# Kernel optimization log

Measured on AMD Instinct MI355X. Metric: run time of the kernel, lower is better.

Reference implementation:

```python
import jax, jax.numpy as jnp
import numpy as np

N_NODES = 100000
N_EDGES = 640000
HIDDEN = 128
OUT = 128


def _graph_conv(x, edge_index, W_rel, b_rel, W_root):
    # PyG GraphConv (aggr='add'):
    #   out[i] = x[i] @ W_root.T + (sum_{(j->i) in E} x[j]) @ W_rel.T + b_rel
    src, dst = edge_index[0], edge_index[1]
    agg = jax.ops.segment_sum(x[src], dst, num_segments=N_NODES)  # [N, d_in]
    return x @ W_root.T + agg @ W_rel.T + b_rel


def setup_inputs() -> dict:
    key = jax.random.key(0)
    ks = jax.random.split(key, 10)
    x = jax.random.normal(ks[0], (N_NODES, HIDDEN), dtype=jnp.float32)
    edge_index = jax.random.randint(ks[1], (2, N_EDGES), 0, N_NODES, dtype=jnp.int64)
    s = 1.0 / np.sqrt(HIDDEN)
    def w(k, o, i):
        return jax.random.normal(k, (o, i), dtype=jnp.float32) * s
    return {
        "x": x,
        "edge_index": edge_index,
        "W_rel0": w(ks[2], HIDDEN, HIDDEN), "b0": jnp.zeros((HIDDEN,), jnp.float32), "W_root0": w(ks[3], HIDDEN, HIDDEN),
        "W_rel1": w(ks[4], HIDDEN, HIDDEN), "b1": jnp.zeros((HIDDEN,), jnp.float32), "W_root1": w(ks[5], HIDDEN, HIDDEN),
        "W_rel2": w(ks[6], OUT, HIDDEN),    "b2": jnp.zeros((OUT,), jnp.float32),    "W_root2": w(ks[7], OUT, HIDDEN),
    }


def reference(x, edge_index, W_rel0, b0, W_root0, W_rel1, b1, W_root1, W_rel2, b2, W_root2):
    h = jax.nn.relu(_graph_conv(x, edge_index, W_rel0, b0, W_root0))
    h = jax.nn.relu(_graph_conv(h, edge_index, W_rel1, b1, W_root1))
    h = _graph_conv(h, edge_index, W_rel2, b2, W_root2)  # no ReLU on end_conv
    return h
```

## Files before the change

kernel.cpp:

```cpp
#include <hip/hip_runtime.h>

constexpr int HID = 128;

typedef __attribute__((ext_vector_type(8))) short bf16x8;
typedef __attribute__((ext_vector_type(4))) float f32x4;

__device__ __forceinline__ unsigned short f2bf(float f) {
    unsigned int u = __float_as_uint(f);
    u += 0x7fffu + ((u >> 16) & 1u);
    return (unsigned short)(u >> 16);
}
__device__ __forceinline__ float bf_lo(unsigned int v) { return __uint_as_float(v << 16); }
__device__ __forceinline__ float bf_hi(unsigned int v) { return __uint_as_float(v & 0xffff0000u); }

__device__ __forceinline__ void gload16(const void* g, void* l) {
    __builtin_amdgcn_global_load_lds(
        (const __attribute__((address_space(1))) void*)g,
        (__attribute__((address_space(3))) void*)l, 16, 0, 0);
}

__global__ __launch_bounds__(256) void cvt_x_k(
    const float* __restrict__ in, unsigned short* __restrict__ out, int n4)
{
    const int i = blockIdx.x * 256 + threadIdx.x;
    if (i >= n4) return;
    const float4 v = reinterpret_cast<const float4*>(in)[i];
    ushort4 o;
    o.x = f2bf(v.x); o.y = f2bf(v.y); o.z = f2bf(v.z); o.w = f2bf(v.w);
    reinterpret_cast<ushort4*>(out)[i] = o;
}

struct WPtrs { const float* s[6]; unsigned short* d[6]; };
__global__ __launch_bounds__(256) void cvt_w_k(WPtrs p)
{
    const int which = blockIdx.y;
    const int i = blockIdx.x * 256 + threadIdx.x;
    if (i >= (HID * HID) / 4) return;
    const float4 v = reinterpret_cast<const float4*>(p.s[which])[i];
    ushort4 o;
    o.x = f2bf(v.x); o.y = f2bf(v.y); o.z = f2bf(v.z); o.w = f2bf(v.w);
    reinterpret_cast<ushort4*>(p.d[which])[i] = o;
}

__global__ __launch_bounds__(256) void hist_k(
    const int* __restrict__ dst, int* __restrict__ deg, int nEdges)
{
    const int i = blockIdx.x * blockDim.x + threadIdx.x;
    if (i < nEdges) atomicAdd(&deg[dst[i]], 1);
}

__global__ __launch_bounds__(256) void scan1_k(
    const int* __restrict__ deg, int* __restrict__ part,
    int* __restrict__ blockSums, int n)
{
    __shared__ int s[256];
    const int t = threadIdx.x;
    const int i = blockIdx.x * 1024 + t * 4;
    const int e0 = (i + 0 < n) ? deg[i + 0] : 0;
    const int e1 = (i + 1 < n) ? deg[i + 1] : 0;
    const int e2 = (i + 2 < n) ? deg[i + 2] : 0;
    const int e3 = (i + 3 < n) ? deg[i + 3] : 0;
    const int local = e0 + e1 + e2 + e3;
    s[t] = local;
    __syncthreads();
    for (int off = 1; off < 256; off <<= 1) {
        int v = 0;
        if (t >= off) v = s[t - off];
        __syncthreads();
        if (t >= off) s[t] += v;
        __syncthreads();
    }
    const int incl = s[t];
    int excl = incl - local;
    if (t == 255) blockSums[blockIdx.x] = incl;
    if (i + 0 < n) part[i + 0] = excl; excl += e0;
    if (i + 1 < n) part[i + 1] = excl; excl += e1;
    if (i + 2 < n) part[i + 2] = excl; excl += e2;
    if (i + 3 < n) part[i + 3] = excl;
}

__global__ __launch_bounds__(128) void scan2_k(int* __restrict__ blockSums, int nb)
{
    __shared__ int s[128];
    const int t = threadIdx.x;
    const int v = (t < nb) ? blockSums[t] : 0;
    s[t] = v;
    __syncthreads();
    for (int off = 1; off < 128; off <<= 1) {
        int u = 0;
        if (t >= off) u = s[t - off];
        __syncthreads();
        if (t >= off) s[t] += u;
        __syncthreads();
    }
    if (t < nb) blockSums[t] = s[t] - v;
}

__global__ __launch_bounds__(256) void scan3_k(
    const int* __restrict__ part, const int* __restrict__ blockSums,
    int* __restrict__ rowStart, int n, int nEdges)
{
    const int i = blockIdx.x * blockDim.x + threadIdx.x;
    if (i < n) rowStart[i] = part[i] + blockSums[i >> 10];
    if (i == n) rowStart[n] = nEdges;
}

__global__ __launch_bounds__(256) void fill_k(
    const int* __restrict__ src, const int* __restrict__ dst,
    int* __restrict__ cursor, int* __restrict__ eSrc, int nEdges)
{
    const int i = blockIdx.x * blockDim.x + threadIdx.x;
    if (i < nEdges) {
        const int pos = atomicAdd(&cursor[dst[i]], 1);
        eSrc[pos] = src[i];
    }
}

__global__ __launch_bounds__(256) void gather_agg_k(
    const unsigned short* __restrict__ feat,
    const int*            __restrict__ rowStart,
    const int*            __restrict__ eSrc,
    unsigned short*       __restrict__ agg,
    int nNodes)
{
    const int node = (int)((blockIdx.x * blockDim.x + threadIdx.x) >> 6);
    if (node >= nNodes) return;
    const int lane = threadIdx.x & 63;
    const int beg = rowStart[node];
    const int end = rowStart[node + 1];
    const size_t colOff = (size_t)lane * 2;

    float ax = 0.f, ay = 0.f;

    for (int base = beg; base < end; base += 64) {
        const int cnt = min(64, end - base);
        const int si = eSrc[base + min(lane, cnt - 1)];

        int j = 0;
        for (; j + 8 <= cnt; j += 8) {
            unsigned int v[8];
#pragma unroll
            for (int q = 0; q < 8; ++q) {
                const int s = __shfl(si, j + q, 64);
                v[q] = *reinterpret_cast<const unsigned int*>(feat + (size_t)s * HID + colOff);
            }
#pragma unroll
            for (int q = 0; q < 8; ++q) { ax += bf_lo(v[q]); ay += bf_hi(v[q]); }
        }
        if (j + 4 <= cnt) {
            unsigned int v[4];
#pragma unroll
            for (int q = 0; q < 4; ++q) {
                const int s = __shfl(si, j + q, 64);
                v[q] = *reinterpret_cast<const unsigned int*>(feat + (size_t)s * HID + colOff);
            }
#pragma unroll
            for (int q = 0; q < 4; ++q) { ax += bf_lo(v[q]); ay += bf_hi(v[q]); }
            j += 4;
        }
        if (j + 2 <= cnt) {
            const int s0 = __shfl(si, j, 64);
            const int s1 = __shfl(si, j + 1, 64);
            const unsigned int v0 = *reinterpret_cast<const unsigned int*>(feat + (size_t)s0 * HID + colOff);
            const unsigned int v1 = *reinterpret_cast<const unsigned int*>(feat + (size_t)s1 * HID + colOff);
            ax += bf_lo(v0) + bf_lo(v1);
            ay += bf_hi(v0) + bf_hi(v1);
            j += 2;
        }
        if (j < cnt) {
            const int s = __shfl(si, j, 64);
            const unsigned int v = *reinterpret_cast<const unsigned int*>(feat + (size_t)s * HID + colOff);
            ax += bf_lo(v);
            ay += bf_hi(v);
        }
    }

    const unsigned int packed = (unsigned int)f2bf(ax) | ((unsigned int)f2bf(ay) << 16);
    *reinterpret_cast<unsigned int*>(agg + (size_t)node * HID + colOff) = packed;
}

template <int MODE>
__global__ __launch_bounds__(256) void gemm_mfma_k(
    const unsigned short* __restrict__ X,
    const unsigned short* __restrict__ AGG,
    const unsigned short* __restrict__ Wroot,
    const unsigned short* __restrict__ Wrel,
    const float*          __restrict__ bias,
    void*                 __restrict__ OUTv,
    int nRows)
{
    __shared__ unsigned short Xs[128 * 64];
    __shared__ unsigned short Ws[128 * 64];

    const int tid  = threadIdx.x;
    const int lane = tid & 63;
    const int w    = tid >> 6;
    const int row0 = blockIdx.x * 128;

    const int wr = w >> 1, wc = w & 1;
    const int R0 = wr * 64, C0 = wc * 64;
    const int lr = lane & 15, lk = lane >> 4;
    const int swz = (lr & 7) << 4;

    const int rsub    = lane >> 3;
    const int srcColB = (((lane & 7) ^ rsub) << 4);
    const int stHalf  = w & 1;
    const int rowMax  = nRows - 1;

    f32x4 acc[4][4];
#pragma unroll
    for (int m = 0; m < 4; ++m)
#pragma unroll
        for (int n = 0; n < 4; ++n) acc[m][n] = f32x4{0.f, 0.f, 0.f, 0.f};

#pragma unroll
    for (int half = 0; half < 2; ++half) {
        const unsigned short* F  = half ? AGG  : X;
        const unsigned short* Wm = half ? Wrel : Wroot;
#pragma unroll
        for (int c = 0; c < 2; ++c) {
            const int k0 = c * 64;
            if (w < 2) {
#pragma unroll
                for (int q = 0; q < 8; ++q) {
                    const int row = stHalf * 64 + q * 8 + rsub;
                    const int gr  = min(row0 + row, rowMax);
                    const char* g = (const char*)(F + (size_t)gr * HID + k0) + srcColB;
                    unsigned short* l = Xs + (stHalf * 64 + q * 8) * 64;
                    gload16(g, l);
                }
            } else {
#pragma unroll
                for (int q = 0; q < 8; ++q) {
                    const int row = stHalf * 64 + q * 8 + rsub;
                    const char* g = (const char*)(Wm + (size_t)row * HID + k0) + srcColB;
                    unsigned short* l = Ws + (stHalf * 64 + q * 8) * 64;
                    gload16(g, l);
                }
            }
            __syncthreads();

#pragma unroll
            for (int ks = 0; ks < 2; ++ks) {
                bf16x8 af[4], bfr[4];
                const int kB = (ks * 64 + lk * 16) ^ swz;
#pragma unroll
                for (int m = 0; m < 4; ++m) {
                    const int row = R0 + m * 16 + lr;
                    af[m] = *reinterpret_cast<const bf16x8*>((const char*)Xs + row * 128 + kB);
                }
#pragma unroll
                for (int n = 0; n < 4; ++n) {
                    const int col = C0 + n * 16 + lr;
                    bfr[n] = *reinterpret_cast<const bf16x8*>((const char*)Ws + col * 128 + kB);
                }
#pragma unroll
                for (int m = 0; m < 4; ++m)
#pragma unroll
                    for (int n = 0; n < 4; ++n)
                        acc[m][n] = __builtin_amdgcn_mfma_f32_16x16x32_bf16(
                            af[m], bfr[n], acc[m][n], 0, 0, 0);
            }
            __syncthreads();
        }
    }

    float bv[4];
#pragma unroll
    for (int n = 0; n < 4; ++n) bv[n] = bias[C0 + n * 16 + lr];

#pragma unroll
    for (int m = 0; m < 4; ++m) {
        const int rbase = row0 + R0 + m * 16 + lk * 4;
#pragma unroll
        for (int j = 0; j < 4; ++j) {
            const int r = rbase + j;
            if (r < nRows) {
#pragma unroll
                for (int n = 0; n < 4; ++n) {
                    const int col = C0 + n * 16 + lr;
                    float v = acc[m][n][j] + bv[n];
                    if (MODE == 0) {
                        v = fmaxf(v, 0.f);
                        ((unsigned short*)OUTv)[(size_t)r * HID + col] = f2bf(v);
                    } else {
                        ((float*)OUTv)[(size_t)r * HID + col] = v;
                    }
                }
            }
        }
    }
}

extern "C" void kernel_launch(void* const* d_in, const int* in_sizes, int n_in,
                              void* d_out, int out_size, void* d_ws, size_t ws_size,
                              hipStream_t stream)
{
    const float* x      = (const float*)d_in[0];
    const int*   ei     = (const int*)  d_in[1];
    const float* Wrel0  = (const float*)d_in[2];
    const float* b0     = (const float*)d_in[3];
    const float* Wroot0 = (const float*)d_in[4];
    const float* Wrel1  = (const float*)d_in[5];
    const float* b1     = (const float*)d_in[6];
    const float* Wroot1 = (const float*)d_in[7];
    const float* Wrel2  = (const float*)d_in[8];
    const float* b2     = (const float*)d_in[9];
    const float* Wroot2 = (const float*)d_in[10];

    const int nNodes = in_sizes[0] / HID;
    const int nEdges = in_sizes[1] / 2;
    const int* srcI = ei;
    const int* dstI = ei + nEdges;
    const size_t nF = (size_t)nNodes * HID;

    float* OUT = (float*)d_out;

    unsigned short* xb   = (unsigned short*)d_ws;
    unsigned short* hA   = xb + nF;
    unsigned short* hB   = hA + nF;
    unsigned short* aggb = hB + nF;
    unsigned short* wb   = aggb + nF;
    int* deg       = (int*)(wb + 6 * HID * HID);
    int* part      = deg + nNodes;
    int* rowStart  = part + nNodes;
    int* cursor    = rowStart + nNodes + 1;
    int* blockSums = cursor + nNodes;
    int* eSrc      = blockSums + 128;

    unsigned short* Wrel0b  = wb + 0 * HID * HID;
    unsigned short* Wroot0b = wb + 1 * HID * HID;
    unsigned short* Wrel1b  = wb + 2 * HID * HID;
    unsigned short* Wroot1b = wb + 3 * HID * HID;
    unsigned short* Wrel2b  = wb + 4 * HID * HID;
    unsigned short* Wroot2b = wb + 5 * HID * HID;

    cvt_x_k<<<(int)((nF / 4 + 255) / 256), 256, 0, stream>>>(x, xb, (int)(nF / 4));
    WPtrs wp;
    wp.s[0] = Wrel0;  wp.d[0] = Wrel0b;
    wp.s[1] = Wroot0; wp.d[1] = Wroot0b;
    wp.s[2] = Wrel1;  wp.d[2] = Wrel1b;
    wp.s[3] = Wroot1; wp.d[3] = Wroot1b;
    wp.s[4] = Wrel2;  wp.d[4] = Wrel2b;
    wp.s[5] = Wroot2; wp.d[5] = Wroot2b;
    cvt_w_k<<<dim3(16, 6), 256, 0, stream>>>(wp);

    const int nb = (nNodes + 1023) / 1024;
    hipMemsetAsync(deg, 0, (size_t)nNodes * sizeof(int), stream);
    hist_k<<<(nEdges + 255) / 256, 256, 0, stream>>>(dstI, deg, nEdges);
    scan1_k<<<nb, 256, 0, stream>>>(deg, part, blockSums, nNodes);
    scan2_k<<<1, 128, 0, stream>>>(blockSums, nb);
    scan3_k<<<(nNodes + 256) / 256, 256, 0, stream>>>(part, blockSums, rowStart, nNodes, nEdges);
    hipMemcpyAsync(cursor, rowStart, (size_t)nNodes * sizeof(int),
                   hipMemcpyDeviceToDevice, stream);
    fill_k<<<(nEdges + 255) / 256, 256, 0, stream>>>(srcI, dstI, cursor, eSrc, nEdges);

    const int aGrid = (int)(((size_t)nNodes * 64 + 255) / 256);
    const int gGrid = (nNodes + 127) / 128;

    gather_agg_k<<<aGrid, 256, 0, stream>>>(xb, rowStart, eSrc, aggb, nNodes);
    gemm_mfma_k<0><<<gGrid, 256, 0, stream>>>(xb, aggb, Wroot0b, Wrel0b, b0, hA, nNodes);

    gather_agg_k<<<aGrid, 256, 0, stream>>>(hA, rowStart, eSrc, aggb, nNodes);
    gemm_mfma_k<0><<<gGrid, 256, 0, stream>>>(hA, aggb, Wroot1b, Wrel1b, b1, hB, nNodes);

    gather_agg_k<<<aGrid, 256, 0, stream>>>(hB, rowStart, eSrc, aggb, nNodes);
    gemm_mfma_k<1><<<gGrid, 256, 0, stream>>>(hB, aggb, Wroot2b, Wrel2b, b2, OUT, nNodes);
}
```

Baseline: 247.5 us.

## Double-buffer GEMM LDS tiles and fold cursor copy into scan kernel

The GEMM kernel now keeps two LDS buffers for the X and W tiles and issues the global-to-LDS loads for the next K chunk before computing on the current one. It relies on explicit vmcnt waits and raw s_barrier calls in place of a sync after every chunk. Separately, scan3 now writes the cursor array directly, which removes a device-to-device memcpy. The cost is double the LDS use per block, which may lower occupancy, and a hand-managed wait count that has to match the number of outstanding loads.

New measurement: 244.4 us (median of 2 runs). No clear change (-1.3%).

```diff
diff --git a/kernel.cpp b/kernel.cpp
--- a/kernel.cpp
+++ b/kernel.cpp
@@ -98,10 +98,14 @@
 
 __global__ __launch_bounds__(256) void scan3_k(
     const int* __restrict__ part, const int* __restrict__ blockSums,
-    int* __restrict__ rowStart, int n, int nEdges)
+    int* __restrict__ rowStart, int* __restrict__ cursor, int n, int nEdges)
 {
     const int i = blockIdx.x * blockDim.x + threadIdx.x;
-    if (i < n) rowStart[i] = part[i] + blockSums[i >> 10];
+    if (i < n) {
+        const int v = part[i] + blockSums[i >> 10];
+        rowStart[i] = v;
+        cursor[i]   = v;
+    }
     if (i == n) rowStart[n] = nEdges;
 }
 
@@ -177,6 +181,29 @@
 
     const unsigned int packed = (unsigned int)f2bf(ax) | ((unsigned int)f2bf(ay) << 16);
     *reinterpret_cast<unsigned int*>(agg + (size_t)node * HID + colOff) = packed;
+}
+
+__device__ __forceinline__ void stage_tile(
+    const unsigned short* __restrict__ F, const unsigned short* __restrict__ Wm,
+    unsigned short* XsBuf, unsigned short* WsBuf,
+    int w, int stHalf, int rsub, int srcColB, int k0, int row0, int rowMax)
+{
+    if (w < 2) {
+#pragma unroll
+        for (int q = 0; q < 8; ++q) {
+            const int row = stHalf * 64 + q * 8 + rsub;
+            const int gr  = min(row0 + row, rowMax);
+            gload16((const char*)(F + (size_t)gr * HID + k0) + srcColB,
+                    XsBuf + (stHalf * 64 + q * 8) * 64);
+        }
+    } else {
+#pragma unroll
+        for (int q = 0; q < 8; ++q) {
+            const int row = stHalf * 64 + q * 8 + rsub;
+            gload16((const char*)(Wm + (size_t)row * HID + k0) + srcColB,
+                    WsBuf + (stHalf * 64 + q * 8) * 64);
+        }
+    }
 }
 
 template <int MODE>
@@ -189,8 +216,8 @@
     void*                 __restrict__ OUTv,
     int nRows)
 {
-    __shared__ unsigned short Xs[128 * 64];
-    __shared__ unsigned short Ws[128 * 64];
+    __shared__ unsigned short Xs[2][128 * 64];
+    __shared__ unsigned short Ws[2][128 * 64];
 
     const int tid  = threadIdx.x;
     const int lane = tid & 63;
@@ -213,56 +240,44 @@
 #pragma unroll
         for (int n = 0; n < 4; ++n) acc[m][n] = f32x4{0.f, 0.f, 0.f, 0.f};
 
-#pragma unroll
-    for (int half = 0; half < 2; ++half) {
-        const unsigned short* F  = half ? AGG  : X;
-        const unsigned short* Wm = half ? Wrel : Wroot;
-#pragma unroll
-        for (int c = 0; c < 2; ++c) {
-            const int k0 = c * 64;
-            if (w < 2) {
-#pragma unroll
-                for (int q = 0; q < 8; ++q) {
-                    const int row = stHalf * 64 + q * 8 + rsub;
-                    const int gr  = min(row0 + row, rowMax);
-                    const char* g = (const char*)(F + (size_t)gr * HID + k0) + srcColB;
-                    unsigned short* l = Xs + (stHalf * 64 + q * 8) * 64;
-                    gload16(g, l);
-                }
-            } else {
-#pragma unroll
-                for (int q = 0; q < 8; ++q) {
-                    const int row = stHalf * 64 + q * 8 + rsub;
-                    const char* g = (const char*)(Wm + (size_t)row * HID + k0) + srcColB;
-                    unsigned short* l = Ws + (stHalf * 64 + q * 8) * 64;
-                    gload16(g, l);
-                }
-            }
-            __syncthreads();
-
-#pragma unroll
-            for (int ks = 0; ks < 2; ++ks) {
-                bf16x8 af[4], bfr[4];
-                const int kB = (ks * 64 + lk * 16) ^ swz;
-#pragma unroll
-                for (int m = 0; m < 4; ++m) {
-                    const int row = R0 + m * 16 + lr;
-                    af[m] = *reinterpret_cast<const bf16x8*>((const char*)Xs + row * 128 + kB);
-                }
-#pragma unroll
-                for (int n = 0; n < 4; ++n) {
-                    const int col = C0 + n * 16 + lr;
-                    bfr[n] = *reinterpret_cast<const bf16x8*>((const char*)Ws + col * 128 + kB);
-                }
-#pragma unroll
-                for (int m = 0; m < 4; ++m)
-#pragma unroll
-                    for (int n = 0; n < 4; ++n)
-                        acc[m][n] = __builtin_amdgcn_mfma_f32_16x16x32_bf16(
-                            af[m], bfr[n], acc[m][n], 0, 0, 0);
-            }
-            __syncthreads();
-        }
+    stage_tile(X, Wroot, Xs[0], Ws[0], w, stHalf, rsub, srcColB, 0, row0, rowMax);
+
+#pragma unroll
+    for (int t = 0; t < 4; ++t) {
+        const int cur = t & 1;
+        if (t < 3) {
+            const unsigned short* Fn = (t + 1 < 2) ? X : AGG;
+            const unsigned short* Wn = (t + 1 < 2) ? Wroot : Wrel;
+            stage_tile(Fn, Wn, Xs[cur ^ 1], Ws[cur ^ 1],
+                       w, stHalf, rsub, srcColB, ((t + 1) & 1) * 64, row0, rowMax);
+            asm volatile("s_waitcnt vmcnt(8)" ::: "memory");
+        } else {
+            asm volatile("s_waitcnt vmcnt(0)" ::: "memory");
+        }
+        __builtin_amdgcn_s_barrier();
+
+#pragma unroll
+        for (int ks = 0; ks < 2; ++ks) {
+            bf16x8 af[4], bfr[4];
+            const int kB = (ks * 64 + lk * 16) ^ swz;
+#pragma unroll
+            for (int m = 0; m < 4; ++m) {
+                const int row = R0 + m * 16 + lr;
+                af[m] = *reinterpret_cast<const bf16x8*>((const char*)Xs[cur] + row * 128 + kB);
+            }
+#pragma unroll
+            for (int n = 0; n < 4; ++n) {
+                const int col = C0 + n * 16 + lr;
+                bfr[n] = *reinterpret_cast<const bf16x8*>((const char*)Ws[cur] + col * 128 + kB);
+            }
+#pragma unroll
+            for (int m = 0; m < 4; ++m)
+#pragma unroll
+                for (int n = 0; n < 4; ++n)
+                    acc[m][n] = __builtin_amdgcn_mfma_f32_16x16x32_bf16(
+                        af[m], bfr[n], acc[m][n], 0, 0, 0);
+        }
+        if (t < 3) __builtin_amdgcn_s_barrier();
     }
 
     float bv[4];
@@ -350,9 +365,7 @@
     hist_k<<<(nEdges + 255) / 256, 256, 0, stream>>>(dstI, deg, nEdges);
     scan1_k<<<nb, 256, 0, stream>>>(deg, part, blockSums, nNodes);
     scan2_k<<<1, 128, 0, stream>>>(blockSums, nb);
-    scan3_k<<<(nNodes + 256) / 256, 256, 0, stream>>>(part, blockSums, rowStart, nNodes, nEdges);
-    hipMemcpyAsync(cursor, rowStart, (size_t)nNodes * sizeof(int),
-                   hipMemcpyDeviceToDevice, stream);
+    scan3_k<<<(nNodes + 256) / 256, 256, 0, stream>>>(part, blockSums, rowStart, cursor, nNodes, nEdges);
     fill_k<<<(nEdges + 255) / 256, 256, 0, stream>>>(srcI, dstI, cursor, eSrc, nEdges);
 
     const int aGrid = (int)(((size_t)nNodes * 64 + 255) / 256);
```
